# Optimization experiments

Measured on AMD Instinct MI355X. Metric: run time of the kernel, lower is better.

## Reference

```python
import jax, jax.numpy as jnp
import numpy as np

C, H, M = 32, 128, 256  # input_dim, hidden_dim, mlp_hidden_dim
B, L = 128, 200          # batch, num spline intervals (W = L+1 grid times)


def setup_inputs() -> dict:
    key = jax.random.key(0)
    ks = jax.random.split(key, 6)
    coeffs = jax.random.normal(ks[0], (B, L, 4 * C), jnp.float32)
    W1 = jax.random.normal(ks[1], (H, M), jnp.float32) / np.sqrt(H).astype(np.float32)
    b1 = jnp.zeros((M,), jnp.float32)
    # last layer of CDEFunc.net is scaled by 0.1 in the original module
    W2 = jax.random.normal(ks[2], (M, H * C), jnp.float32) * np.float32(0.1 / np.sqrt(M))
    b2 = jnp.zeros((H * C,), jnp.float32)
    Wz = jax.random.normal(ks[3], (C, H), jnp.float32) / np.sqrt(C).astype(np.float32)
    bz = jnp.zeros((H,), jnp.float32)
    gamma = jnp.ones((H,), jnp.float32)
    beta = jnp.zeros((H,), jnp.float32)
    return dict(coeffs=coeffs, W1=W1, b1=b1, W2=W2, b2=b2, Wz=Wz, bz=bz,
                gamma=gamma, beta=beta)


def _field(z, W1, b1, W2, b2):
    # z: (..., H) -> tanh(MLP(z)) reshaped to (..., H, C)
    h = jax.nn.relu(z @ W1 + b1)
    f = jnp.tanh(h @ W2 + b2)
    return f.reshape(z.shape[:-1] + (H, C))


def reference(coeffs, W1, b1, W2, b2, Wz, bz, gamma, beta):
    # coeffs layout per torchcde: concat([a, b, two_c, three_d], -1), each (B,L,C)
    a, b, two_c, three_d = jnp.split(coeffs, 4, axis=-1)
    # spline derivative at t = interval_start + frac: b + (two_c + three_d*frac)*frac
    # torchcde bucketize convention: exact grid time i>=1 falls in interval i-1 at frac=1;
    # t=0 falls in interval 0 at frac=0.
    d_end = b + two_c + three_d                           # deriv at frac=1, (B,L,C)
    d_grid = jnp.concatenate([b[:, :1], d_end], axis=1)   # (B, L+1, C) deriv at grid times
    d13 = b + two_c * (1.0 / 3.0) + three_d * (1.0 / 9.0)  # frac = 1/3
    d23 = b + two_c * (2.0 / 3.0) + three_d * (4.0 / 9.0)  # frac = 2/3

    z0 = a[:, 0] @ Wz + bz  # x0 = X(0) = a[:,0]; z0_proj

    def g(z, d):  # controlled vector field: f(z) . dX/dt
        return jnp.einsum('bhc,bc->bh', _field(z, W1, b1, W2, b2), d)

    def step(z, ds):  # torchdiffeq 'rk4' = 3/8 rule, dt = 1
        d0, da, db_, d1 = ds
        k1 = g(z, d0)
        k2 = g(z + k1 * (1.0 / 3.0), da)
        k3 = g(z + (k2 - k1 * (1.0 / 3.0)), db_)
        k4 = g(z + (k1 - k2 + k3), d1)
        zn = z + (k1 + 3.0 * (k2 + k3) + k4) * 0.125
        return zn, zn

    ds = (jnp.swapaxes(d_grid[:, :-1], 0, 1),  # (L,B,C) deriv at t0 of each interval
          jnp.swapaxes(d13, 0, 1),
          jnp.swapaxes(d23, 0, 1),
          jnp.swapaxes(d_grid[:, 1:], 0, 1))   # deriv at t1 of each interval
    _, z_rest = jax.lax.scan(step, z0, ds)
    z_wbh = jnp.concatenate([z0[None], z_rest], axis=0)   # (W, B, H)

    field = _field(z_wbh, W1, b1, W2, b2)                 # (W, B, H, C)
    xdot = jnp.swapaxes(d_grid, 0, 1)                     # (W, B, C)
    sd = jnp.einsum('wbhc,wbc->wbh', field, xdot)
    sd = jnp.swapaxes(sd, 0, 1)                           # (B, W, H)
    mu = jnp.mean(sd, axis=-1, keepdims=True)
    var = jnp.var(sd, axis=-1, keepdims=True)
    sd = (sd - mu) * jax.lax.rsqrt(var + 1e-5) * gamma + beta
    return jnp.clip(sd, -1000.0, 1000.0)
```

## Files before the change

kernel.cpp:

```cpp
#include <hip/hip_runtime.h>
#include <hip/hip_bf16.h>


#define AGENT __HIP_MEMORY_SCOPE_AGENT

__device__ __forceinline__ float ldA(const float* p) {
  return __hip_atomic_load(p, __ATOMIC_RELAXED, AGENT);
}
__device__ __forceinline__ void stA(float* p, float v) {
  __hip_atomic_store(p, v, __ATOMIC_RELAXED, AGENT);
}
__device__ __forceinline__ float4 ld4A(const float* p) {
  float4 a;
  asm volatile("global_load_dwordx4 %0, %1, off sc0 sc1\n\t"
               "s_waitcnt vmcnt(0)"
               : "=v"(a) : "v"(p) : "memory");
  return a;
}
__device__ __forceinline__ void ld4A2(const float* p0, const float* p1,
                                      float4& a, float4& b) {
  asm volatile("global_load_dwordx4 %0, %2, off sc0 sc1\n\t"
               "global_load_dwordx4 %1, %3, off sc0 sc1\n\t"
               "s_waitcnt vmcnt(0)"
               : "=&v"(a), "=&v"(b) : "v"(p0), "v"(p1) : "memory");
}

struct Lds {
  float4 zins4[8][32];
  float4 w1t4[8][32];
  float  hs[2048];
  float  ds[8][32];
  float  kacc2[8][1024];
  float  psum[8][32];
  float  kout[8][4];
  float  lnsum[8][32];
  float  lnsq[8][32];
  float  lnmv[8][2];
};

__global__ void __launch_bounds__(256) ncde_kernel(
    const float* __restrict__ coeffs, const float* __restrict__ W1,
    const float* __restrict__ b1, const float* __restrict__ W2,
    const float* __restrict__ b2, const float* __restrict__ Wz,
    const float* __restrict__ bz, const float* __restrict__ gam,
    const float* __restrict__ bet, float* __restrict__ out,
    float* __restrict__ ws)
{
  __shared__ Lds L;
  const int t  = threadIdx.x;
  const int cl = blockIdx.x >> 5;
  const int jp = blockIdx.x & 31;

  unsigned* slots = (unsigned*)ws + cl * 64;
  unsigned* genp  = slots + 32;
  unsigned  ph = 0;

  float* kb = ws + 1024 + cl * 4096;
  float* hb = ws + 1024 + 16 * 4096 + cl * 2048;

  const int zrow = t >> 5;
  const int zseg = t & 31;
  const int brow = cl * 8 + zrow;

  {
    const int mj = t >> 5, hc = t & 31;
    float4 v;
    v.x = W1[(hc * 4 + 0) * 256 + jp * 8 + mj];
    v.y = W1[(hc * 4 + 1) * 256 + jp * 8 + mj];
    v.z = W1[(hc * 4 + 2) * 256 + jp * 8 + mj];
    v.w = W1[(hc * 4 + 3) * 256 + jp * 8 + mj];
    L.w1t4[mj][hc ^ mj] = v;
  }

  float zr_[4];
  {
    const float* arow = coeffs + (size_t)brow * 25600;
    #pragma unroll
    for (int i = 0; i < 4; ++i) {
      int h = zseg * 4 + i;
      float acc = bz[h];
      for (int c = 0; c < 32; ++c) acc += arow[c] * Wz[c * 128 + h];
      zr_[i] = acc;
    }
  }

  auto cbar = [&]() {
    __syncthreads();
    asm volatile("s_waitcnt vmcnt(0)" ::: "memory");
    ++ph;
    if (t == 0) __hip_atomic_store(&slots[jp], ph, __ATOMIC_RELAXED, AGENT);
    if (jp == 0) {
      if (t < 32) {
        while (__hip_atomic_load(&slots[t], __ATOMIC_RELAXED, AGENT) < ph)
          __builtin_amdgcn_s_sleep(1);
        if (t == 0) __hip_atomic_store(genp, ph, __ATOMIC_RELAXED, AGENT);
      }
    } else if (t == 0) {
      while (__hip_atomic_load(genp, __ATOMIC_RELAXED, AGENT) < ph)
        __builtin_amdgcn_s_sleep(1);
    }
    __syncthreads();
  };

  auto stage = [&](int l, int s) {
    {
      int lidx; float f = 0.f; bool bonly = false;
      if (s == 0) { if (l == 0) { lidx = 0; bonly = true; } else { lidx = l - 1; f = 1.f; } }
      else if (s == 1) { lidx = l; f = 1.f / 3.f; }
      else if (s == 2) { lidx = l; f = 2.f / 3.f; }
      else             { lidx = l; f = 1.f; }
      const float* cp = coeffs + (size_t)brow * 25600 + (size_t)lidx * 128;
      float bco = cp[32 + zseg];
      L.ds[zrow][zseg] = bonly ? bco : bco + (cp[64 + zseg] + cp[96 + zseg] * f) * f;
    }
    {
      int idx4 = zrow * 128 + zseg * 4;
      float4 zv = make_float4(zr_[0], zr_[1], zr_[2], zr_[3]);
      if (s == 1) {
        float4 k1 = ld4A(kb + idx4);
        zv.x += (1.f/3.f)*k1.x; zv.y += (1.f/3.f)*k1.y;
        zv.z += (1.f/3.f)*k1.z; zv.w += (1.f/3.f)*k1.w;
      } else if (s == 2) {
        float4 k1, k2; ld4A2(kb + idx4, kb + 1024 + idx4, k1, k2);
        zv.x += k2.x - (1.f/3.f)*k1.x; zv.y += k2.y - (1.f/3.f)*k1.y;
        zv.z += k2.z - (1.f/3.f)*k1.z; zv.w += k2.w - (1.f/3.f)*k1.w;
      } else if (s == 3) {
        float4 k1, k2; ld4A2(kb + idx4, kb + 1024 + idx4, k1, k2);
        float4 k3 = ld4A(kb + 2048 + idx4);
        zv.x += k1.x - k2.x + k3.x; zv.y += k1.y - k2.y + k3.y;
        zv.z += k1.z - k2.z + k3.z; zv.w += k1.w - k2.w + k3.w;
      }
      L.zins4[zrow][zseg ^ (zrow * 4)] = zv;
    }
    __syncthreads();
    if (t < 64) {
      int r = t >> 3, mj = t & 7;
      float acc = 0.f;
      #pragma unroll 8
      for (int hc = 0; hc < 32; ++hc) {
        float4 z4 = L.zins4[r][hc ^ (r * 4)];
        float4 w4 = L.w1t4[mj][hc ^ mj];
        acc += z4.x * w4.x + z4.y * w4.y + z4.z * w4.z + z4.w * w4.w;
      }
      acc += b1[jp * 8 + mj];
      acc = fmaxf(acc, 0.f);
      stA(hb + r * 256 + jp * 8 + mj, acc);
    }
    cbar();
    {
      float4 a, b;
      ld4A2(hb + t * 4, hb + 1024 + t * 4, a, b);
      *(float4*)&L.hs[t * 4] = a;
      *(float4*)&L.hs[1024 + t * 4] = b;
    }
    __syncthreads();
    {
      const int col4 = t & 31, kq = t >> 5;
      const float* w2b = W2 + (size_t)(kq * 32) * 4096 + jp * 128 + col4 * 4;
      float4 acc[8];
      #pragma unroll
      for (int r = 0; r < 8; ++r) acc[r] = make_float4(0.f, 0.f, 0.f, 0.f);
      float4 n0 = *(const float4*)(w2b);
      float4 n1 = *(const float4*)(w2b + 4096);
      float4 n2 = *(const float4*)(w2b + 2 * 4096);
      float4 n3 = *(const float4*)(w2b + 3 * 4096);
      for (int mo = 0; mo < 8; ++mo) {
        float4 w0 = n0, w1v = n1, w2v = n2, w3v = n3;
        if (mo < 7) {
          const float* nb = w2b + (size_t)(mo + 1) * 4 * 4096;
          n0 = *(const float4*)(nb);
          n1 = *(const float4*)(nb + 4096);
          n2 = *(const float4*)(nb + 2 * 4096);
          n3 = *(const float4*)(nb + 3 * 4096);
        }
        #pragma unroll
        for (int r = 0; r < 8; ++r) {
          float4 h4 = *(const float4*)&L.hs[r * 256 + (kq * 8 + mo) * 4];
          acc[r].x += h4.x * w0.x + h4.y * w1v.x + h4.z * w2v.x + h4.w * w3v.x;
          acc[r].y += h4.x * w0.y + h4.y * w1v.y + h4.z * w2v.y + h4.w * w3v.y;
          acc[r].z += h4.x * w0.z + h4.y * w1v.z + h4.z * w2v.z + h4.w * w3v.z;
          acc[r].w += h4.x * w0.w + h4.y * w1v.w + h4.z * w2v.w + h4.w * w3v.w;
        }
      }
      #pragma unroll
      for (int r = 0; r < 8; ++r) {
        float* kp = &L.kacc2[kq][r * 128 + col4];
        kp[0] = acc[r].x; kp[32] = acc[r].y; kp[64] = acc[r].z; kp[96] = acc[r].w;
      }
    }
    __syncthreads();
    {
      float4* k4p = (float4*)&L.kacc2[0][0];
      float4 sv = k4p[t];
      #pragma unroll
      for (int kq = 1; kq < 8; ++kq) {
        float4 v = k4p[kq * 256 + t];
        sv.x += v.x; sv.y += v.y; sv.z += v.z; sv.w += v.w;
      }
      k4p[t] = sv;
    }
    __syncthreads();
    {
      int r = t >> 5, g = t & 31;
      float lsum = 0.f;
      #pragma unroll
      for (int i = 0; i < 4; ++i) {
        int col = g * 4 + i;
        float pre = L.kacc2[0][r * 128 + i * 32 + g] + b2[jp * 128 + col];
        float ax = fabsf(pre);
        float e = __expf(-2.f * ax);
        float th = (1.f - e) * __builtin_amdgcn_rcpf(1.f + e);
        th = (pre < 0.f) ? -th : th;
        lsum += th * L.ds[r][col & 31];
      }
      L.psum[r][g] = lsum;
    }
    __syncthreads();
    if (t < 32) {
      int r = t >> 2, hl = t & 3;
      float s0 = 0.f;
      #pragma unroll
      for (int g = 0; g < 8; ++g) s0 += L.psum[r][hl * 8 + g];
      L.kout[r][hl] = s0;
      stA(kb + s * 1024 + r * 128 + jp * 4 + hl, s0);
    }
    cbar();
  };

  auto lnorm = [&](int w) {
    {
      float4 v = ld4A(kb + zrow * 128 + zseg * 4);
      L.lnsum[zrow][zseg] = v.x + v.y + v.z + v.w;
      L.lnsq[zrow][zseg]  = v.x*v.x + v.y*v.y + v.z*v.z + v.w*v.w;
    }
    __syncthreads();
    if (t < 8) {
      float s0 = 0.f, q0 = 0.f;
      #pragma unroll
      for (int j = 0; j < 32; ++j) { s0 += L.lnsum[t][j]; q0 += L.lnsq[t][j]; }
      float mu = s0 * (1.f / 128.f);
      float var = q0 * (1.f / 128.f) - mu * mu;
      L.lnmv[t][0] = mu;
      L.lnmv[t][1] = rsqrtf(var + 1e-5f);
    }
    __syncthreads();
    if (t < 32) {
      int r = t >> 2, hl = t & 3, h = jp * 4 + hl;
      float x = L.kout[r][hl];
      float y = (x - L.lnmv[r][0]) * L.lnmv[r][1] * gam[h] + bet[h];
      y = fminf(fmaxf(y, -1000.f), 1000.f);
      out[(size_t)(cl * 8 + r) * 25728 + (size_t)w * 128 + h] = y;
    }
    __syncthreads();
  };

  for (int l = 0; l < 200; ++l) {
    stage(l, 0);
    lnorm(l);
    stage(l, 1);
    stage(l, 2);
    stage(l, 3);
    {
      int idx4 = zrow * 128 + zseg * 4;
      float4 k1, k2, k3, k4;
      ld4A2(kb + idx4,        kb + 1024 + idx4, k1, k2);
      ld4A2(kb + 2048 + idx4, kb + 3072 + idx4, k3, k4);
      zr_[0] += 0.125f * (k1.x + 3.f * (k2.x + k3.x) + k4.x);
      zr_[1] += 0.125f * (k1.y + 3.f * (k2.y + k3.y) + k4.y);
      zr_[2] += 0.125f * (k1.z + 3.f * (k2.z + k3.z) + k4.z);
      zr_[3] += 0.125f * (k1.w + 3.f * (k2.w + k3.w) + k4.w);
    }
  }
  stage(200, 0);
  lnorm(200);
}

extern "C" void kernel_launch(void* const* d_in, const int* in_sizes, int n_in,
                              void* d_out, int out_size, void* d_ws, size_t ws_size,
                              hipStream_t stream) {
  (void)in_sizes; (void)n_in; (void)out_size; (void)ws_size;
  const float* coeffs = (const float*)d_in[0];
  const float* W1     = (const float*)d_in[1];
  const float* b1     = (const float*)d_in[2];
  const float* W2     = (const float*)d_in[3];
  const float* b2     = (const float*)d_in[4];
  const float* Wz     = (const float*)d_in[5];
  const float* bz     = (const float*)d_in[6];
  const float* gam    = (const float*)d_in[7];
  const float* bet    = (const float*)d_in[8];
  float* out = (float*)d_out;
  float* ws  = (float*)d_ws;

  hipMemsetAsync(d_ws, 0, 4096, stream);
  ncde_kernel<<<dim3(512), dim3(256), 0, stream>>>(coeffs, W1, b1, W2, b2, Wz, bz,
                                                   gam, bet, out, ws);
}
```

Measured before the change: 15.80 ms.

## Compute full first MLP layer redundantly per block to drop a grid barrier

Each block now computes the whole first layer (z@W1, all 256 hidden units for its 8 rows) locally with a 4-way k-split in shared memory, instead of computing an 8-column slice and exchanging it through global memory with a cluster-wide barrier. This removes one of the two cross-block barriers per RK stage, at the cost of every block doing 32x redundant layer-1 work and re-reading all of W1 each stage. The k1 buffer is double-buffered by interval parity so the stage-0 write for the next step does not overwrite data still being read.

```diff
diff --git a/kernel.cpp b/kernel.cpp
--- a/kernel.cpp
+++ b/kernel.cpp
@@ -4,9 +4,6 @@
 
 #define AGENT __HIP_MEMORY_SCOPE_AGENT
 
-__device__ __forceinline__ float ldA(const float* p) {
-  return __hip_atomic_load(p, __ATOMIC_RELAXED, AGENT);
-}
 __device__ __forceinline__ void stA(float* p, float v) {
   __hip_atomic_store(p, v, __ATOMIC_RELAXED, AGENT);
 }
@@ -24,19 +21,6 @@
                "s_waitcnt vmcnt(0)"
                : "=&v"(a), "=&v"(b) : "v"(p0), "v"(p1) : "memory");
 }
-
-struct Lds {
-  float4 zins4[8][32];
-  float4 w1t4[8][32];
-  float  hs[2048];
-  float  ds[8][32];
-  float  kacc2[8][1024];
-  float  psum[8][32];
-  float  kout[8][4];
-  float  lnsum[8][32];
-  float  lnsq[8][32];
-  float  lnmv[8][2];
-};
 
 __global__ void __launch_bounds__(256) ncde_kernel(
     const float* __restrict__ coeffs, const float* __restrict__ W1,
@@ -46,7 +30,14 @@
     const float* __restrict__ bet, float* __restrict__ out,
     float* __restrict__ ws)
 {
-  __shared__ Lds L;
+  __shared__ float zs[8][136];
+  __shared__ float pacc[8192];
+  __shared__ float hs[2048];
+  __shared__ float dsv[8][32];
+  __shared__ float psum[8][32];
+  __shared__ float kout[8][4];
+  __shared__ float lnsum[8][32], lnsq[8][32], lnmv[8][2];
+
   const int t  = threadIdx.x;
   const int cl = blockIdx.x >> 5;
   const int jp = blockIdx.x & 31;
@@ -55,22 +46,14 @@
   unsigned* genp  = slots + 32;
   unsigned  ph = 0;
 
-  float* kb = ws + 1024 + cl * 4096;
-  float* hb = ws + 1024 + 16 * 4096 + cl * 2048;
+  float* kbc = ws + 1024 + cl * 5120;
 
   const int zrow = t >> 5;
   const int zseg = t & 31;
   const int brow = cl * 8 + zrow;
 
-  {
-    const int mj = t >> 5, hc = t & 31;
-    float4 v;
-    v.x = W1[(hc * 4 + 0) * 256 + jp * 8 + mj];
-    v.y = W1[(hc * 4 + 1) * 256 + jp * 8 + mj];
-    v.z = W1[(hc * 4 + 2) * 256 + jp * 8 + mj];
-    v.w = W1[(hc * 4 + 3) * 256 + jp * 8 + mj];
-    L.w1t4[mj][hc ^ mj] = v;
-  }
+  const float  b1v = b1[t];
+  const float4 b2v = *(const float4*)&b2[jp * 128 + (t & 31) * 4];
 
   float zr_[4];
   {
@@ -103,6 +86,7 @@
   };
 
   auto stage = [&](int l, int s) {
+    const int p1 = l & 1;
     {
       int lidx; float f = 0.f; bool bonly = false;
       if (s == 0) { if (l == 0) { lidx = 0; bonly = true; } else { lidx = l - 1; f = 1.f; } }
@@ -111,47 +95,67 @@
       else             { lidx = l; f = 1.f; }
       const float* cp = coeffs + (size_t)brow * 25600 + (size_t)lidx * 128;
       float bco = cp[32 + zseg];
-      L.ds[zrow][zseg] = bonly ? bco : bco + (cp[64 + zseg] + cp[96 + zseg] * f) * f;
-    }
-    {
+      dsv[zrow][zseg] = bonly ? bco : bco + (cp[64 + zseg] + cp[96 + zseg] * f) * f;
+
       int idx4 = zrow * 128 + zseg * 4;
       float4 zv = make_float4(zr_[0], zr_[1], zr_[2], zr_[3]);
       if (s == 1) {
-        float4 k1 = ld4A(kb + idx4);
+        float4 k1 = ld4A(kbc + p1 * 1024 + idx4);
         zv.x += (1.f/3.f)*k1.x; zv.y += (1.f/3.f)*k1.y;
         zv.z += (1.f/3.f)*k1.z; zv.w += (1.f/3.f)*k1.w;
       } else if (s == 2) {
-        float4 k1, k2; ld4A2(kb + idx4, kb + 1024 + idx4, k1, k2);
+        float4 k1, k2; ld4A2(kbc + p1 * 1024 + idx4, kbc + 2 * 1024 + idx4, k1, k2);
         zv.x += k2.x - (1.f/3.f)*k1.x; zv.y += k2.y - (1.f/3.f)*k1.y;
         zv.z += k2.z - (1.f/3.f)*k1.z; zv.w += k2.w - (1.f/3.f)*k1.w;
       } else if (s == 3) {
-        float4 k1, k2; ld4A2(kb + idx4, kb + 1024 + idx4, k1, k2);
-        float4 k3 = ld4A(kb + 2048 + idx4);
+        float4 k1, k2; ld4A2(kbc + p1 * 1024 + idx4, kbc + 2 * 1024 + idx4, k1, k2);
+        float4 k3 = ld4A(kbc + 3 * 1024 + idx4);
         zv.x += k1.x - k2.x + k3.x; zv.y += k1.y - k2.y + k3.y;
         zv.z += k1.z - k2.z + k3.z; zv.w += k1.w - k2.w + k3.w;
       }
-      L.zins4[zrow][zseg ^ (zrow * 4)] = zv;
-    }
-    __syncthreads();
-    if (t < 64) {
-      int r = t >> 3, mj = t & 7;
-      float acc = 0.f;
-      #pragma unroll 8
-      for (int hc = 0; hc < 32; ++hc) {
-        float4 z4 = L.zins4[r][hc ^ (r * 4)];
-        float4 w4 = L.w1t4[mj][hc ^ mj];
-        acc += z4.x * w4.x + z4.y * w4.y + z4.z * w4.z + z4.w * w4.w;
-      }
-      acc += b1[jp * 8 + mj];
-      acc = fmaxf(acc, 0.f);
-      stA(hb + r * 256 + jp * 8 + mj, acc);
-    }
-    cbar();
-    {
-      float4 a, b;
-      ld4A2(hb + t * 4, hb + 1024 + t * 4, a, b);
-      *(float4*)&L.hs[t * 4] = a;
-      *(float4*)&L.hs[1024 + t * 4] = b;
+      *(float4*)&zs[zrow][zseg * 4] = zv;
+    }
+    __syncthreads();
+    {
+      const int cg = t & 63, kq2 = t >> 6;
+      const float* w1p = W1 + (size_t)(kq2 * 32) * 256 + cg * 4;
+      float4 acc[8];
+      #pragma unroll
+      for (int r = 0; r < 8; ++r) acc[r] = make_float4(0.f, 0.f, 0.f, 0.f);
+      float4 n0 = *(const float4*)(w1p);
+      float4 n1 = *(const float4*)(w1p + 256);
+      float4 n2 = *(const float4*)(w1p + 512);
+      float4 n3 = *(const float4*)(w1p + 768);
+      for (int mo = 0; mo < 8; ++mo) {
+        float4 w0 = n0, w1v = n1, w2v = n2, w3v = n3;
+        if (mo < 7) {
+          const float* nb = w1p + (size_t)(mo + 1) * 1024;
+          n0 = *(const float4*)(nb);
+          n1 = *(const float4*)(nb + 256);
+          n2 = *(const float4*)(nb + 512);
+          n3 = *(const float4*)(nb + 768);
+        }
+        #pragma unroll
+        for (int r = 0; r < 8; ++r) {
+          float4 zq = *(const float4*)&zs[r][kq2 * 32 + mo * 4];
+          acc[r].x += zq.x * w0.x + zq.y * w1v.x + zq.z * w2v.x + zq.w * w3v.x;
+          acc[r].y += zq.x * w0.y + zq.y * w1v.y + zq.z * w2v.y + zq.w * w3v.y;
+          acc[r].z += zq.x * w0.z + zq.y * w1v.z + zq.z * w2v.z + zq.w * w3v.z;
+          acc[r].w += zq.x * w0.w + zq.y * w1v.w + zq.z * w2v.w + zq.w * w3v.w;
+        }
+      }
+      #pragma unroll
+      for (int r = 0; r < 8; ++r)
+        *(float4*)&pacc[kq2 * 2048 + r * 256 + cg * 4] = acc[r];
+    }
+    __syncthreads();
+    {
+      #pragma unroll
+      for (int i = 0; i < 8; ++i) {
+        int idx = i * 256 + t;
+        float v = pacc[idx] + pacc[2048 + idx] + pacc[4096 + idx] + pacc[6144 + idx];
+        hs[idx] = fmaxf(v + b1v, 0.f);
+      }
     }
     __syncthreads();
     {
@@ -175,7 +179,7 @@
         }
         #pragma unroll
         for (int r = 0; r < 8; ++r) {
-          float4 h4 = *(const float4*)&L.hs[r * 256 + (kq * 8 + mo) * 4];
+          float4 h4 = *(const float4*)&hs[r * 256 + (kq * 8 + mo) * 4];
           acc[r].x += h4.x * w0.x + h4.y * w1v.x + h4.z * w2v.x + h4.w * w3v.x;
           acc[r].y += h4.x * w0.y + h4.y * w1v.y + h4.z * w2v.y + h4.w * w3v.y;
           acc[r].z += h4.x * w0.z + h4.y * w1v.z + h4.z * w2v.z + h4.w * w3v.z;
@@ -184,13 +188,13 @@
       }
       #pragma unroll
       for (int r = 0; r < 8; ++r) {
-        float* kp = &L.kacc2[kq][r * 128 + col4];
+        float* kp = &pacc[kq * 1024 + r * 128 + col4];
         kp[0] = acc[r].x; kp[32] = acc[r].y; kp[64] = acc[r].z; kp[96] = acc[r].w;
       }
     }
     __syncthreads();
     {
-      float4* k4p = (float4*)&L.kacc2[0][0];
+      float4* k4p = (float4*)pacc;
       float4 sv = k4p[t];
       #pragma unroll
       for (int kq = 1; kq < 8; ++kq) {
@@ -202,52 +206,56 @@
     __syncthreads();
     {
       int r = t >> 5, g = t & 31;
+      float pre0 = pacc[r * 128 + 0 * 32 + g] + b2v.x;
+      float pre1 = pacc[r * 128 + 1 * 32 + g] + b2v.y;
+      float pre2 = pacc[r * 128 + 2 * 32 + g] + b2v.z;
+      float pre3 = pacc[r * 128 + 3 * 32 + g] + b2v.w;
       float lsum = 0.f;
       #pragma unroll
       for (int i = 0; i < 4; ++i) {
-        int col = g * 4 + i;
-        float pre = L.kacc2[0][r * 128 + i * 32 + g] + b2[jp * 128 + col];
+        float pre = (i == 0) ? pre0 : (i == 1) ? pre1 : (i == 2) ? pre2 : pre3;
         float ax = fabsf(pre);
         float e = __expf(-2.f * ax);
         float th = (1.f - e) * __builtin_amdgcn_rcpf(1.f + e);
         th = (pre < 0.f) ? -th : th;
-        lsum += th * L.ds[r][col & 31];
-      }
-      L.psum[r][g] = lsum;
+        lsum += th * dsv[r][(g * 4 + i) & 31];
+      }
+      psum[r][g] = lsum;
     }
     __syncthreads();
     if (t < 32) {
       int r = t >> 2, hl = t & 3;
       float s0 = 0.f;
       #pragma unroll
-      for (int g = 0; g < 8; ++g) s0 += L.psum[r][hl * 8 + g];
-      L.kout[r][hl] = s0;
-      stA(kb + s * 1024 + r * 128 + jp * 4 + hl, s0);
+      for (int g = 0; g < 8; ++g) s0 += psum[r][hl * 8 + g];
+      kout[r][hl] = s0;
+      int buf = (s == 0) ? p1 : (s + 1);
+      stA(kbc + buf * 1024 + r * 128 + jp * 4 + hl, s0);
     }
     cbar();
   };
 
   auto lnorm = [&](int w) {
     {
-      float4 v = ld4A(kb + zrow * 128 + zseg * 4);
-      L.lnsum[zrow][zseg] = v.x + v.y + v.z + v.w;
-      L.lnsq[zrow][zseg]  = v.x*v.x + v.y*v.y + v.z*v.z + v.w*v.w;
+      float4 v = ld4A(kbc + (w & 1) * 1024 + zrow * 128 + zseg * 4);
+      lnsum[zrow][zseg] = v.x + v.y + v.z + v.w;
+      lnsq[zrow][zseg]  = v.x*v.x + v.y*v.y + v.z*v.z + v.w*v.w;
     }
     __syncthreads();
     if (t < 8) {
       float s0 = 0.f, q0 = 0.f;
       #pragma unroll
-      for (int j = 0; j < 32; ++j) { s0 += L.lnsum[t][j]; q0 += L.lnsq[t][j]; }
+      for (int j = 0; j < 32; ++j) { s0 += lnsum[t][j]; q0 += lnsq[t][j]; }
       float mu = s0 * (1.f / 128.f);
       float var = q0 * (1.f / 128.f) - mu * mu;
-      L.lnmv[t][0] = mu;
-      L.lnmv[t][1] = rsqrtf(var + 1e-5f);
+      lnmv[t][0] = mu;
+      lnmv[t][1] = rsqrtf(var + 1e-5f);
     }
     __syncthreads();
     if (t < 32) {
       int r = t >> 2, hl = t & 3, h = jp * 4 + hl;
-      float x = L.kout[r][hl];
-      float y = (x - L.lnmv[r][0]) * L.lnmv[r][1] * gam[h] + bet[h];
+      float x = kout[r][hl];
+      float y = (x - lnmv[r][0]) * lnmv[r][1] * gam[h] + bet[h];
       y = fminf(fmaxf(y, -1000.f), 1000.f);
       out[(size_t)(cl * 8 + r) * 25728 + (size_t)w * 128 + h] = y;
     }
@@ -263,8 +271,8 @@
     {
       int idx4 = zrow * 128 + zseg * 4;
       float4 k1, k2, k3, k4;
-      ld4A2(kb + idx4,        kb + 1024 + idx4, k1, k2);
-      ld4A2(kb + 2048 + idx4, kb + 3072 + idx4, k3, k4);
+      ld4A2(kbc + (l & 1) * 1024 + idx4, kbc + 2 * 1024 + idx4, k1, k2);
+      ld4A2(kbc + 3 * 1024 + idx4,       kbc + 4 * 1024 + idx4, k3, k4);
       zr_[0] += 0.125f * (k1.x + 3.f * (k2.x + k3.x) + k4.x);
       zr_[1] += 0.125f * (k1.y + 3.f * (k2.y + k3.y) + k4.y);
       zr_[2] += 0.125f * (k1.z + 3.f * (k2.z + k3.z) + k4.z);
```

Result: slower. 22.89 ms (+44.9%).
